# Kernel tuning notes

Hardware: AMD Instinct MI355X
Metric: run time of the kernel (lower is better)

The kernel has to match this reference:

```python
import jax, jax.numpy as jnp
import numpy as np

B, T, D, H, A = 64, 4096, 128, 512, 18


def setup_inputs() -> dict:
    key = jax.random.key(0)
    ks = jax.random.split(key, 6)
    obses = jax.random.normal(ks[0], (B, T, D), dtype=jnp.float32)
    init_c = jnp.zeros((B, H), dtype=jnp.float32)
    init_h = jnp.zeros((B, H), dtype=jnp.float32)
    # flax LSTMCell: dense_i (no bias) on x, dense_h (bias) on h, 4 gates (i,f,g,o)
    Wi = jax.random.normal(ks[1], (D, 4 * H), dtype=jnp.float32) * (1.0 / np.sqrt(D))
    Wh = jax.random.normal(ks[2], (H, 4 * H), dtype=jnp.float32) * (1.0 / np.sqrt(H))
    b = jnp.zeros((4 * H,), dtype=jnp.float32)
    Wv = jax.random.normal(ks[3], (H, A), dtype=jnp.float32) * (1.0 / np.sqrt(H))
    bv = jnp.zeros((A,), dtype=jnp.float32)
    return {"obses": obses, "init_c": init_c, "init_h": init_h,
            "Wi": Wi, "Wh": Wh, "b": b, "Wv": Wv, "bv": bv}


def reference(obses, init_c, init_h, Wi, Wh, b, Wv, bv):
    # Precompute all input projections in one big GEMM: (B,T,4H)
    x_proj = jnp.einsum('btd,dg->btg', obses, Wi) + b
    x_proj_t = jnp.swapaxes(x_proj, 0, 1)  # time-major (T,B,4H)

    def step(carry, xt):
        c, h = carry
        gates = xt + h @ Wh  # (B,4H)
        i, f, g, o = jnp.split(gates, 4, axis=-1)
        i = jax.nn.sigmoid(i)
        f = jax.nn.sigmoid(f)
        g = jnp.tanh(g)
        o = jax.nn.sigmoid(o)
        new_c = f * c + i * g
        new_h = o * jnp.tanh(new_c)
        return (new_c, new_h), new_h

    (c, h), hs = jax.lax.scan(step, (init_c, init_h), x_proj_t)
    lstm_out = jnp.swapaxes(hs, 0, 1)  # (B,T,H)
    qs = lstm_out @ Wv + bv  # (B,T,A)
    return ((c, h), qs)
```

## Files before the change

kernel.cpp:

```cpp
#include <hip/hip_runtime.h>
#include <stdint.h>
#include <stddef.h>


#define B_   64
#define T_   4096
#define D_   128
#define H_   512
#define G4_  2048
#define A_   18
#define QOFF (2 * B_ * H_)
#define BIAS 1.5f

typedef float f32x4  __attribute__((ext_vector_type(4)));
typedef short bf16x8 __attribute__((ext_vector_type(8)));
typedef unsigned long long u64;
#define MFMA __builtin_amdgcn_mfma_f32_16x16x32_bf16

#define QD_IDX(g,w)  (((g) * 4 + (w)) * 16)
#define CTL_DWORDS   1024
#define HS_OFF       65536
#define TLIM         400000000ull
#define SMASK        0x8000800080008000ull

__device__ __forceinline__ short f2bf(float x) {
    union { float f; uint32_t u; } v; v.f = x;
    uint32_t r = (v.u + 0x7fffu + ((v.u >> 16) & 1u)) >> 16;
    return (short)(uint16_t)r;
}
__device__ __forceinline__ float bf2f(short s) {
    union { uint32_t u; float f; } v; v.u = ((uint32_t)(uint16_t)s) << 16;
    return v.f;
}
__device__ __forceinline__ float sigm(float x) {
    return __builtin_amdgcn_rcpf(1.0f + __builtin_amdgcn_exp2f(-1.4426950408889634f * x));
}
__device__ __forceinline__ float tanh_(float x) {
    return 2.0f * __builtin_amdgcn_rcpf(1.0f + __builtin_amdgcn_exp2f(-2.8853900817779268f * x)) - 1.0f;
}

__global__ void lstm_fill(unsigned* __restrict__ ctl, uint4* __restrict__ hs4,
                          int nchunks) {
    int idx = blockIdx.x * blockDim.x + threadIdx.x;
    int nt  = gridDim.x * blockDim.x;
    for (int i = idx; i < CTL_DWORDS; i += nt) ctl[i] = 0u;
    const uint4 v = {0x80008000u, 0x80008000u, 0x80008000u, 0x80008000u};
    for (int i = idx; i < nchunks; i += nt) hs4[i] = v;
}

__global__ void lstm_init0(const float* __restrict__ init_h,
                           short* __restrict__ hs, int R) {
    int idx = blockIdx.x * blockDim.x + threadIdx.x;
    int nt  = gridDim.x * blockDim.x;
    for (int e = idx; e < B_ * H_; e += nt) {
        int row = e >> 9, col = e & 511;
        int g = row >> 3, r8 = row & 7;
        hs[(size_t)g * R * 4096 + (size_t)r8 * 512 + col] = f2bf(init_h[e] + BIAS);
    }
}

__global__ void __launch_bounds__(256, 1) lstm_main(
    const float* __restrict__ obses, const float* __restrict__ init_c,
    const float* __restrict__ Wi,    const float* __restrict__ Wh,
    const float* __restrict__ bvec,  const float* __restrict__ Wv,
    const float* __restrict__ bv,    float* __restrict__ out,
    unsigned* ctl, short* hs, int R, int lg2R)
{
    const int bid = blockIdx.x;
    const int w   = threadIdx.x >> 6;
    const int l   = threadIdx.x & 63;
    const int n   = l & 15;
    const int kg  = l >> 4;
    const int Rm  = R - 1;
    const unsigned long long t_start = __builtin_amdgcn_s_memrealtime();
    bool tmo = false;

    if (bid < 128) {
        __shared__ u64 lds_h[2][8 * 132];
        const int g = bid & 7;
        const int k = bid >> 3;
        short* hsg = hs + (size_t)g * R * 4096;

        const int cw  = k * 32 + w * 8;
        const int gc0 = (n & 3) * 512 + cw + (n >> 2);
        const int gc1 = gc0 + 4;

        bf16x8 whA0[16], whA1[16], wiA0[4], wiA1[4];
        float ws0 = 0.f, ws1 = 0.f;
#pragma unroll
        for (int ch = 0; ch < 16; ++ch) {
            bf16x8 v0, v1;
#pragma unroll
            for (int j = 0; j < 8; ++j) {
                const size_t kr = (size_t)(ch * 32 + kg * 8 + j) * G4_;
                short s0 = f2bf(Wh[kr + gc0]); v0[j] = s0; ws0 += bf2f(s0);
                short s1 = f2bf(Wh[kr + gc1]); v1[j] = s1; ws1 += bf2f(s1);
            }
            whA0[ch] = v0; whA1[ch] = v1;
        }
#pragma unroll
        for (int ch = 0; ch < 4; ++ch) {
            bf16x8 v0, v1;
#pragma unroll
            for (int j = 0; j < 8; ++j) {
                const size_t kr = (size_t)(ch * 32 + kg * 8 + j) * G4_;
                v0[j] = f2bf(Wi[kr + gc0]);
                v1[j] = f2bf(Wi[kr + gc1]);
            }
            wiA0[ch] = v0; wiA1[ch] = v1;
        }
        ws0 += __shfl_xor(ws0, 16); ws0 += __shfl_xor(ws0, 32);
        ws1 += __shfl_xor(ws1, 16); ws1 += __shfl_xor(ws1, 32);
        const float b0v = bvec[gc0], b1v = bvec[gc1];
        const float sP0 = b0v - BIAS * ws0, sM0 = b0v + BIAS * ws0;
        const float sP1 = b1v - BIAS * ws1, sM1 = b1v + BIAS * ws1;
        f32x4 sdP0, sdM0, sdP1, sdM1;
#pragma unroll
        for (int r = 0; r < 4; ++r) {
            sdP0[r] = __shfl(sP0, kg * 4 + r); sdM0[r] = __shfl(sM0, kg * 4 + r);
            sdP1[r] = __shfl(sP1, kg * 4 + r); sdM1[r] = __shfl(sM1, kg * 4 + r);
        }

        float cst0 = (n < 8) ? init_c[(size_t)(g * 8 + n) * H_ + cw + kg]     : 0.f;
        float cst1 = (n < 8) ? init_c[(size_t)(g * 8 + n) * H_ + cw + 4 + kg] : 0.f;
        float hl0 = 0.f, hl1 = 0.f;

        f32x4 oraw[8];
        if (n < 8) {
            const float* src = obses + ((size_t)(g * 8 + n) * T_ + 0) * D_ + kg * 8;
#pragma unroll
            for (int ch = 0; ch < 4; ++ch) {
                oraw[2 * ch]     = *(const f32x4*)(src + ch * 32);
                oraw[2 * ch + 1] = *(const f32x4*)(src + ch * 32 + 4);
            }
        }

        const int prow = l >> 3;
        const int pcol = w * 32 + (l & 7);

        const int CHK  = R >> 2;
        const int CHKm = CHK - 1;

        for (int t = 0; t < T_ && !tmo; ++t) {
            if ((t & CHKm) == 0) {
                const int need = t + CHK + 4 - R;
                if (need > 0) {
                    int spin = 0; bool ok;
                    do {
                        int p = 0x7fffffff;
                        if (l < 4)
                            p = 1 + l + 4 * (int)__hip_atomic_load(ctl + QD_IDX(g, l),
                                    __ATOMIC_RELAXED, __HIP_MEMORY_SCOPE_AGENT);
                        ok = (__all(p >= need) != 0);
                        if (!ok && ((++spin) & 63) == 0 &&
                            (__builtin_amdgcn_s_memrealtime() - t_start) > TLIM) { tmo = true; break; }
                    } while (!ok);
                    if (tmo) break;
                }
            }

            const bool  pos = (((t >> lg2R) & 1) == 0);
            const float bh1 = (((t + 1) >> lg2R) & 1) ? -BIAS : BIAS;

            bf16x8 obsF[4];
#pragma unroll
            for (int ch = 0; ch < 4; ++ch) {
                bf16x8 v;
                if (n < 8) {
#pragma unroll
                    for (int j = 0; j < 4; ++j) {
                        v[j]     = f2bf(oraw[2 * ch][j]);
                        v[4 + j] = f2bf(oraw[2 * ch + 1][j]);
                    }
                } else {
#pragma unroll
                    for (int j = 0; j < 8; ++j) v[j] = 0;
                }
                obsF[ch] = v;
            }
            if (t + 1 < T_ && n < 8) {
                const float* src = obses + ((size_t)(g * 8 + n) * T_ + (t + 1)) * D_ + kg * 8;
#pragma unroll
                for (int ch = 0; ch < 4; ++ch) {
                    oraw[2 * ch]     = *(const f32x4*)(src + ch * 32);
                    oraw[2 * ch + 1] = *(const f32x4*)(src + ch * 32 + 4);
                }
            }

            f32x4 aE0 = pos ? sdP0 : sdM0;
            f32x4 aE1 = pos ? sdP1 : sdM1;
            f32x4 aO0 = {0.f, 0.f, 0.f, 0.f}, aO1 = {0.f, 0.f, 0.f, 0.f};
            aE0 = MFMA(wiA0[0], obsF[0], aE0, 0, 0, 0);
            aO0 = MFMA(wiA0[1], obsF[1], aO0, 0, 0, 0);
            aE0 = MFMA(wiA0[2], obsF[2], aE0, 0, 0, 0);
            aO0 = MFMA(wiA0[3], obsF[3], aO0, 0, 0, 0);
            aE1 = MFMA(wiA1[0], obsF[0], aE1, 0, 0, 0);
            aO1 = MFMA(wiA1[1], obsF[1], aO1, 0, 0, 0);
            aE1 = MFMA(wiA1[2], obsF[2], aE1, 0, 0, 0);
            aO1 = MFMA(wiA1[3], obsF[3], aO1, 0, 0, 0);

            {
                const u64* hp = (const u64*)(hsg + (size_t)(t & Rm) * 4096)
                                + prow * 128 + pcol;
                const u64 e64 = pos ? 0ull : SMASK;
                u64 q0v, q1v, q2v, q3v;
                int spin = 0;
                for (;;) {
                    q0v = __hip_atomic_load(hp,      __ATOMIC_RELAXED, __HIP_MEMORY_SCOPE_AGENT);
                    q1v = __hip_atomic_load(hp + 8,  __ATOMIC_RELAXED, __HIP_MEMORY_SCOPE_AGENT);
                    q2v = __hip_atomic_load(hp + 16, __ATOMIC_RELAXED, __HIP_MEMORY_SCOPE_AGENT);
                    q3v = __hip_atomic_load(hp + 24, __ATOMIC_RELAXED, __HIP_MEMORY_SCOPE_AGENT);
                    u64 bad = (q0v ^ e64) | (q1v ^ e64) | (q2v ^ e64) | (q3v ^ e64);
                    if (__all((int)((bad & SMASK) == 0ull))) break;
                    if (((++spin) & 255) == 0 &&
                        (__builtin_amdgcn_s_memrealtime() - t_start) > TLIM) { tmo = true; break; }
                }
                if (tmo) break;
                u64* dst = &lds_h[t & 1][prow * 132 + pcol];
                dst[0]  = q0v;
                dst[8]  = q1v;
                dst[16] = q2v;
                dst[24] = q3v;
            }
            __syncthreads();

            const u64* lb = &lds_h[t & 1][n * 132 + kg * 2];
#pragma unroll
            for (int ch = 0; ch < 16; ++ch) {
                union { u64 q[2]; bf16x8 v; } u;
                if (n < 8) { u.q[0] = lb[ch * 8]; u.q[1] = lb[ch * 8 + 1]; }
                else       { u.q[0] = 0ull; u.q[1] = 0ull; }
                if (ch & 1) { aO0 = MFMA(whA0[ch], u.v, aO0, 0, 0, 0);
                              aO1 = MFMA(whA1[ch], u.v, aO1, 0, 0, 0); }
                else        { aE0 = MFMA(whA0[ch], u.v, aE0, 0, 0, 0);
                              aE1 = MFMA(whA1[ch], u.v, aE1, 0, 0, 0); }
            }

            f32x4 x0 = aE0 + aO0, x1 = aE1 + aO1;
            float nc0 = sigm(x0[1]) * cst0 + sigm(x0[0]) * tanh_(x0[2]);
            float nh0 = sigm(x0[3]) * tanh_(nc0);
            float nc1 = sigm(x1[1]) * cst1 + sigm(x1[0]) * tanh_(x1[2]);
            float nh1 = sigm(x1[3]) * tanh_(nc1);
            cst0 = nc0; cst1 = nc1; hl0 = nh0; hl1 = nh1;

            {
                const int slw = (t + 1) & Rm;
                unsigned v = (unsigned)(unsigned short)f2bf(nh0 + bh1) |
                             ((unsigned)(unsigned short)f2bf(nh1 + bh1) << 16);
                unsigned p  = (unsigned)__shfl_xor((int)v, 16);
                unsigned dwA = (v & 0xffffu) | (p << 16);
                unsigned dwB = (v >> 16) | (p & 0xffff0000u);
                unsigned qA = (unsigned)__shfl_xor((int)dwA, 32);
                unsigned qB = (unsigned)__shfl_xor((int)dwB, 32);
                u64 lo = (u64)dwA | ((u64)qA << 32);
                u64 hi = (u64)dwB | ((u64)qB << 32);
                if (kg == 0 && n < 8) {
                    u64* dst = (u64*)(hsg + (size_t)slw * 4096 + (size_t)n * 512 + cw);
                    __hip_atomic_store(dst,     lo, __ATOMIC_RELAXED, __HIP_MEMORY_SCOPE_AGENT);
                    __hip_atomic_store(dst + 1, hi, __ATOMIC_RELAXED, __HIP_MEMORY_SCOPE_AGENT);
                }
            }
        }

        if (n < 8 && !tmo) {
            const size_t brow = (size_t)(g * 8 + n);
            out[brow * H_ + cw + kg]     = cst0;
            out[brow * H_ + cw + 4 + kg] = cst1;
            out[(size_t)B_ * H_ + brow * H_ + cw + kg]     = hl0;
            out[(size_t)B_ * H_ + brow * H_ + cw + 4 + kg] = hl1;
        }
    } else {
        const int g = bid - 128;
        short* hsg = hs + (size_t)g * R * 4096;

        bf16x8 wvF[2][16]; float wvsum[2] = {0.f, 0.f}; float bvv[2];
#pragma unroll
        for (int c = 0; c < 2; ++c) {
            const int a  = c * 16 + n;
            const bool va = (a < A_);
#pragma unroll
            for (int ch = 0; ch < 16; ++ch) {
                bf16x8 v;
#pragma unroll
                for (int j = 0; j < 8; ++j) {
                    short sbf = va ? f2bf(Wv[(size_t)(ch * 32 + kg * 8 + j) * A_ + a]) : (short)0;
                    v[j] = sbf; wvsum[c] += bf2f(sbf);
                }
                wvF[c][ch] = v;
            }
            bvv[c] = va ? bv[a] : 0.f;
        }
#pragma unroll
        for (int c = 0; c < 2; ++c) {
            wvsum[c] += __shfl_xor(wvsum[c], 16);
            wvsum[c] += __shfl_xor(wvsum[c], 32);
        }

        u64 hq[32];
        if (n >= 8) {
#pragma unroll
            for (int i = 0; i < 32; ++i) hq[i] = 0ull;
        }

        unsigned cnt = 0;
        for (int s = 1 + w; s <= T_ && !tmo; s += 4) {
            const float bh = ((s >> lg2R) & 1) ? -BIAS : BIAS;
            const u64 e64 = (bh > 0.f) ? 0ull : SMASK;
            {
                const u64* hp = (const u64*)(hsg + (size_t)(s & Rm) * 4096)
                                + n * 128 + kg * 2;
                int spin = 0; bool fresh = true;
                do {
                    if (n < 8) {
                        u64 bad = 0;
#pragma unroll
                        for (int ch = 0; ch < 16; ++ch) {
                            hq[2 * ch]     = __hip_atomic_load(hp + ch * 8,     __ATOMIC_RELAXED, __HIP_MEMORY_SCOPE_AGENT);
                            hq[2 * ch + 1] = __hip_atomic_load(hp + ch * 8 + 1, __ATOMIC_RELAXED, __HIP_MEMORY_SCOPE_AGENT);
                        }
#pragma unroll
                        for (int i = 0; i < 32; ++i) bad |= (hq[i] ^ e64);
                        fresh = ((bad & SMASK) == 0ull);
                    }
                    if (__all(fresh)) break;
                    __builtin_amdgcn_s_sleep(2);
                    if (((++spin) & 255) == 0 &&
                        (__builtin_amdgcn_s_memrealtime() - t_start) > TLIM) { tmo = true; break; }
                } while (true);
                if (tmo) break;
            }

            ++cnt;
            asm volatile("" ::: "memory");
            if (l == 0)
                __hip_atomic_store(ctl + QD_IDX(g, w), cnt,
                                   __ATOMIC_RELAXED, __HIP_MEMORY_SCOPE_AGENT);

            const float q0s = bvv[0] - bh * wvsum[0];
            const float q1s = bvv[1] - bh * wvsum[1];
            f32x4 q0 = {q0s, q0s, q0s, q0s};
            f32x4 q1 = {q1s, q1s, q1s, q1s};
#pragma unroll
            for (int ch = 0; ch < 16; ++ch) {
                union { u64 q[2]; bf16x8 v; } u;
                u.q[0] = hq[2 * ch]; u.q[1] = hq[2 * ch + 1];
                q0 = MFMA(u.v, wvF[0][ch], q0, 0, 0, 0);
                q1 = MFMA(u.v, wvF[1][ch], q1, 0, 0, 0);
            }

            const int tau = s - 1;
#pragma unroll
            for (int c = 0; c < 2; ++c) {
                const int a = c * 16 + n;
                if (kg < 2 && a < A_) {
                    const f32x4 q = c ? q1 : q0;
#pragma unroll
                    for (int r = 0; r < 4; ++r)
                        out[QOFF + ((size_t)(g * 8 + kg * 4 + r) * T_ + tau) * A_ + a] = q[r];
                }
            }
        }
    }
}

extern "C" void kernel_launch(void* const* d_in, const int* in_sizes, int n_in,
                              void* d_out, int out_size, void* d_ws, size_t ws_size,
                              hipStream_t stream) {
    const float* obses  = (const float*)d_in[0];
    const float* init_c = (const float*)d_in[1];
    const float* init_h = (const float*)d_in[2];
    const float* Wi     = (const float*)d_in[3];
    const float* Wh     = (const float*)d_in[4];
    const float* b      = (const float*)d_in[5];
    const float* Wv     = (const float*)d_in[6];
    const float* bv     = (const float*)d_in[7];
    float* out = (float*)d_out;

    unsigned* ctl = (unsigned*)d_ws;
    short*    hs  = (short*)((char*)d_ws + HS_OFF);

    int R = 32;
    while (R > 8 && (size_t)HS_OFF + 8ull * R * 8192ull > ws_size) R >>= 1;
    int lg2R = 31 - __builtin_clz((unsigned)R);

    int nchunks = R * 4096;

    hipLaunchKernelGGL(lstm_fill,  dim3(256), dim3(256), 0, stream, ctl, (uint4*)hs, nchunks);
    hipLaunchKernelGGL(lstm_init0, dim3(64),  dim3(256), 0, stream, init_h, hs, R);
    hipLaunchKernelGGL(lstm_main,  dim3(136), dim3(256), 0, stream,
                       obses, init_c, Wi, Wh, b, Wv, bv, out, ctl, hs, R, lg2R);
}
```

Measured before the change: 10.57 ms.

## Pack 16 batch rows per group to fill MFMA N dimension, halve workgroups

```diff
diff --git a/kernel.cpp b/kernel.cpp
--- a/kernel.cpp
+++ b/kernel.cpp
@@ -22,6 +22,7 @@
 #define HS_OFF       65536
 #define TLIM         400000000ull
 #define SMASK        0x8000800080008000ull
+#define SLOT_SH      8192
 
 __device__ __forceinline__ short f2bf(float x) {
     union { float f; uint32_t u; } v; v.f = x;
@@ -54,8 +55,8 @@
     int nt  = gridDim.x * blockDim.x;
     for (int e = idx; e < B_ * H_; e += nt) {
         int row = e >> 9, col = e & 511;
-        int g = row >> 3, r8 = row & 7;
-        hs[(size_t)g * R * 4096 + (size_t)r8 * 512 + col] = f2bf(init_h[e] + BIAS);
+        int g = row >> 4, r16 = row & 15;
+        hs[(size_t)g * R * SLOT_SH + (size_t)r16 * 512 + col] = f2bf(init_h[e] + BIAS);
     }
 }
 
@@ -75,11 +76,11 @@
     const unsigned long long t_start = __builtin_amdgcn_s_memrealtime();
     bool tmo = false;
 
-    if (bid < 128) {
-        __shared__ u64 lds_h[2][8 * 132];
-        const int g = bid & 7;
-        const int k = bid >> 3;
-        short* hsg = hs + (size_t)g * R * 4096;
+    if (bid < 64) {
+        __shared__ u64 lds_h[2][16 * 132];
+        const int g = bid & 3;
+        const int k = bid >> 2;
+        short* hsg = hs + (size_t)g * R * SLOT_SH;
 
         const int cw  = k * 32 + w * 8;
         const int gc0 = (n & 3) * 512 + cw + (n >> 2);
@@ -121,13 +122,13 @@
             sdP1[r] = __shfl(sP1, kg * 4 + r); sdM1[r] = __shfl(sM1, kg * 4 + r);
         }
 
-        float cst0 = (n < 8) ? init_c[(size_t)(g * 8 + n) * H_ + cw + kg]     : 0.f;
-        float cst1 = (n < 8) ? init_c[(size_t)(g * 8 + n) * H_ + cw + 4 + kg] : 0.f;
+        float cst0 = init_c[(size_t)(g * 16 + n) * H_ + cw + kg];
+        float cst1 = init_c[(size_t)(g * 16 + n) * H_ + cw + 4 + kg];
         float hl0 = 0.f, hl1 = 0.f;
 
         f32x4 oraw[8];
-        if (n < 8) {
-            const float* src = obses + ((size_t)(g * 8 + n) * T_ + 0) * D_ + kg * 8;
+        {
+            const float* src = obses + ((size_t)(g * 16 + n) * T_ + 0) * D_ + kg * 8;
 #pragma unroll
             for (int ch = 0; ch < 4; ++ch) {
                 oraw[2 * ch]     = *(const f32x4*)(src + ch * 32);
@@ -135,8 +136,8 @@
             }
         }
 
-        const int prow = l >> 3;
-        const int pcol = w * 32 + (l & 7);
+        const int prow = l >> 2;
+        const int pcol = w * 32 + (l & 3);
 
         const int CHK  = R >> 2;
         const int CHKm = CHK - 1;
@@ -166,20 +167,15 @@
 #pragma unroll
             for (int ch = 0; ch < 4; ++ch) {
                 bf16x8 v;
-                if (n < 8) {
-#pragma unroll
-                    for (int j = 0; j < 4; ++j) {
-                        v[j]     = f2bf(oraw[2 * ch][j]);
-                        v[4 + j] = f2bf(oraw[2 * ch + 1][j]);
-                    }
-                } else {
-#pragma unroll
-                    for (int j = 0; j < 8; ++j) v[j] = 0;
+#pragma unroll
+                for (int j = 0; j < 4; ++j) {
+                    v[j]     = f2bf(oraw[2 * ch][j]);
+                    v[4 + j] = f2bf(oraw[2 * ch + 1][j]);
                 }
                 obsF[ch] = v;
             }
-            if (t + 1 < T_ && n < 8) {
-                const float* src = obses + ((size_t)(g * 8 + n) * T_ + (t + 1)) * D_ + kg * 8;
+            if (t + 1 < T_) {
+                const float* src = obses + ((size_t)(g * 16 + n) * T_ + (t + 1)) * D_ + kg * 8;
 #pragma unroll
                 for (int ch = 0; ch < 4; ++ch) {
                     oraw[2 * ch]     = *(const f32x4*)(src + ch * 32);
@@ -200,27 +196,26 @@
             aO1 = MFMA(wiA1[3], obsF[3], aO1, 0, 0, 0);
 
             {
-                const u64* hp = (const u64*)(hsg + (size_t)(t & Rm) * 4096)
+                const u64* hp = (const u64*)(hsg + (size_t)(t & Rm) * SLOT_SH)
                                 + prow * 128 + pcol;
                 const u64 e64 = pos ? 0ull : SMASK;
-                u64 q0v, q1v, q2v, q3v;
+                u64 q[8];
                 int spin = 0;
                 for (;;) {
-                    q0v = __hip_atomic_load(hp,      __ATOMIC_RELAXED, __HIP_MEMORY_SCOPE_AGENT);
-                    q1v = __hip_atomic_load(hp + 8,  __ATOMIC_RELAXED, __HIP_MEMORY_SCOPE_AGENT);
-                    q2v = __hip_atomic_load(hp + 16, __ATOMIC_RELAXED, __HIP_MEMORY_SCOPE_AGENT);
-                    q3v = __hip_atomic_load(hp + 24, __ATOMIC_RELAXED, __HIP_MEMORY_SCOPE_AGENT);
-                    u64 bad = (q0v ^ e64) | (q1v ^ e64) | (q2v ^ e64) | (q3v ^ e64);
+#pragma unroll
+                    for (int j = 0; j < 8; ++j)
+                        q[j] = __hip_atomic_load(hp + 4 * j, __ATOMIC_RELAXED, __HIP_MEMORY_SCOPE_AGENT);
+                    u64 bad = 0;
+#pragma unroll
+                    for (int j = 0; j < 8; ++j) bad |= (q[j] ^ e64);
                     if (__all((int)((bad & SMASK) == 0ull))) break;
                     if (((++spin) & 255) == 0 &&
                         (__builtin_amdgcn_s_memrealtime() - t_start) > TLIM) { tmo = true; break; }
                 }
                 if (tmo) break;
                 u64* dst = &lds_h[t & 1][prow * 132 + pcol];
-                dst[0]  = q0v;
-                dst[8]  = q1v;
-                dst[16] = q2v;
-                dst[24] = q3v;
+#pragma unroll
+                for (int j = 0; j < 8; ++j) dst[4 * j] = q[j];
             }
             __syncthreads();
 
@@ -228,8 +223,7 @@
 #pragma unroll
             for (int ch = 0; ch < 16; ++ch) {
                 union { u64 q[2]; bf16x8 v; } u;
-                if (n < 8) { u.q[0] = lb[ch * 8]; u.q[1] = lb[ch * 8 + 1]; }
-                else       { u.q[0] = 0ull; u.q[1] = 0ull; }
+                u.q[0] = lb[ch * 8]; u.q[1] = lb[ch * 8 + 1];
                 if (ch & 1) { aO0 = MFMA(whA0[ch], u.v, aO0, 0, 0, 0);
                               aO1 = MFMA(whA1[ch], u.v, aO1, 0, 0, 0); }
                 else        { aE0 = MFMA(whA0[ch], u.v, aE0, 0, 0, 0);
@@ -254,24 +248,24 @@
                 unsigned qB = (unsigned)__shfl_xor((int)dwB, 32);
                 u64 lo = (u64)dwA | ((u64)qA << 32);
                 u64 hi = (u64)dwB | ((u64)qB << 32);
-                if (kg == 0 && n < 8) {
-                    u64* dst = (u64*)(hsg + (size_t)slw * 4096 + (size_t)n * 512 + cw);
+                if (kg == 0) {
+                    u64* dst = (u64*)(hsg + (size_t)slw * SLOT_SH + (size_t)n * 512 + cw);
                     __hip_atomic_store(dst,     lo, __ATOMIC_RELAXED, __HIP_MEMORY_SCOPE_AGENT);
                     __hip_atomic_store(dst + 1, hi, __ATOMIC_RELAXED, __HIP_MEMORY_SCOPE_AGENT);
                 }
             }
         }
 
-        if (n < 8 && !tmo) {
-            const size_t brow = (size_t)(g * 8 + n);
+        if (!tmo) {
+            const size_t brow = (size_t)(g * 16 + n);
             out[brow * H_ + cw + kg]     = cst0;
             out[brow * H_ + cw + 4 + kg] = cst1;
             out[(size_t)B_ * H_ + brow * H_ + cw + kg]     = hl0;
             out[(size_t)B_ * H_ + brow * H_ + cw + 4 + kg] = hl1;
         }
-    } else {
-        const int g = bid - 128;
-        short* hsg = hs + (size_t)g * R * 4096;
+    } else if (bid < 68) {
+        const int g = bid - 64;
+        short* hsg = hs + (size_t)g * R * SLOT_SH;
 
         bf16x8 wvF[2][16]; float wvsum[2] = {0.f, 0.f}; float bvv[2];
 #pragma unroll
@@ -297,31 +291,25 @@
         }
 
         u64 hq[32];
-        if (n >= 8) {
-#pragma unroll
-            for (int i = 0; i < 32; ++i) hq[i] = 0ull;
-        }
 
         unsigned cnt = 0;
         for (int s = 1 + w; s <= T_ && !tmo; s += 4) {
             const float bh = ((s >> lg2R) & 1) ? -BIAS : BIAS;
             const u64 e64 = (bh > 0.f) ? 0ull : SMASK;
             {
-                const u64* hp = (const u64*)(hsg + (size_t)(s & Rm) * 4096)
+                const u64* hp = (const u64*)(hsg + (size_t)(s & Rm) * SLOT_SH)
                                 + n * 128 + kg * 2;
-                int spin = 0; bool fresh = true;
+                int spin = 0; bool fresh;
                 do {
-                    if (n < 8) {
-                        u64 bad = 0;
-#pragma unroll
-                        for (int ch = 0; ch < 16; ++ch) {
-                            hq[2 * ch]     = __hip_atomic_load(hp + ch * 8,     __ATOMIC_RELAXED, __HIP_MEMORY_SCOPE_AGENT);
-                            hq[2 * ch + 1] = __hip_atomic_load(hp + ch * 8 + 1, __ATOMIC_RELAXED, __HIP_MEMORY_SCOPE_AGENT);
-                        }
-#pragma unroll
-                        for (int i = 0; i < 32; ++i) bad |= (hq[i] ^ e64);
-                        fresh = ((bad & SMASK) == 0ull);
+                    u64 bad = 0;
+#pragma unroll
+                    for (int ch = 0; ch < 16; ++ch) {
+                        hq[2 * ch]     = __hip_atomic_load(hp + ch * 8,     __ATOMIC_RELAXED, __HIP_MEMORY_SCOPE_AGENT);
+                        hq[2 * ch + 1] = __hip_atomic_load(hp + ch * 8 + 1, __ATOMIC_RELAXED, __HIP_MEMORY_SCOPE_AGENT);
                     }
+#pragma unroll
+                    for (int i = 0; i < 32; ++i) bad |= (hq[i] ^ e64);
+                    fresh = ((bad & SMASK) == 0ull);
                     if (__all(fresh)) break;
                     __builtin_amdgcn_s_sleep(2);
                     if (((++spin) & 255) == 0 &&
@@ -352,11 +340,11 @@
 #pragma unroll
             for (int c = 0; c < 2; ++c) {
                 const int a = c * 16 + n;
-                if (kg < 2 && a < A_) {
+                if (a < A_) {
                     const f32x4 q = c ? q1 : q0;
 #pragma unroll
                     for (int r = 0; r < 4; ++r)
-                        out[QOFF + ((size_t)(g * 8 + kg * 4 + r) * T_ + tau) * A_ + a] = q[r];
+                        out[QOFF + ((size_t)(g * 16 + kg * 4 + r) * T_ + tau) * A_ + a] = q[r];
                 }
             }
         }
@@ -380,13 +368,13 @@
     short*    hs  = (short*)((char*)d_ws + HS_OFF);
 
     int R = 32;
-    while (R > 8 && (size_t)HS_OFF + 8ull * R * 8192ull > ws_size) R >>= 1;
+    while (R > 8 && (size_t)HS_OFF + 4ull * R * 16384ull > ws_size) R >>= 1;
     int lg2R = 31 - __builtin_clz((unsigned)R);
 
     int nchunks = R * 4096;
 
     hipLaunchKernelGGL(lstm_fill,  dim3(256), dim3(256), 0, stream, ctl, (uint4*)hs, nchunks);
     hipLaunchKernelGGL(lstm_init0, dim3(64),  dim3(256), 0, stream, init_h, hs, R);
-    hipLaunchKernelGGL(lstm_main,  dim3(136), dim3(256), 0, stream,
+    hipLaunchKernelGGL(lstm_main,  dim3(68),  dim3(256), 0, stream,
                        obses, init_c, Wi, Wh, b, Wv, bv, out, ctl, hs, R, lg2R);
 }
```

After: 12.99 ms. +22.8%, slower.
